# Performance work log

Measured on AMD Instinct MI355X. Metric: run time of the kernel, lower is better.

The kernel has to match this reference:

```python
import jax, jax.numpy as jnp
import numpy as np

N_NODES = 50000
N_EDGES = 800000
H = 128       # num_hidden
NUM_INV = 32  # num_inv


def _glorot(key, shape):
    fan_in, fan_out = shape[0], shape[1]
    lim = np.sqrt(6.0 / (fan_in + fan_out)).astype(np.float32)
    return jax.random.uniform(key, shape, jnp.float32, -lim, lim)


def setup_inputs() -> dict:
    key = jax.random.key(0)
    ks = jax.random.split(key, 12)
    x = jax.random.normal(ks[0], (N_NODES, H), jnp.float32)
    adj = jax.random.randint(ks[1], (2, N_EDGES), 0, N_NODES, dtype=jnp.int64)
    inv = jax.random.normal(ks[2], (N_EDGES, NUM_INV), jnp.float32)
    # MessageLayer: message_mlp = Linear(2H+inv -> H), SiLU, Linear(H -> H), SiLU
    Wm1 = _glorot(ks[3], (2 * H + NUM_INV, H)); bm1 = jnp.zeros((H,), jnp.float32)
    Wm2 = _glorot(ks[4], (H, H));               bm2 = jnp.zeros((H,), jnp.float32)
    # edge_inf_mlp = Linear(H -> 1), Sigmoid
    We = _glorot(ks[5], (H, 1));                be = jnp.zeros((1,), jnp.float32)
    # UpdateLayer (num_mes=1): update_mlp = Linear(2H -> H), SiLU, Linear(H -> H)
    Wu1 = _glorot(ks[6], (2 * H, H));           bu1 = jnp.zeros((H,), jnp.float32)
    Wu2 = _glorot(ks[7], (H, H));               bu2 = jnp.zeros((H,), jnp.float32)
    return {"x": x, "adj": adj, "inv": inv,
            "Wm1": Wm1, "bm1": bm1, "Wm2": Wm2, "bm2": bm2,
            "We": We, "be": be,
            "Wu1": Wu1, "bu1": bu1, "Wu2": Wu2, "bu2": bu2}


def reference(x, adj, inv, Wm1, bm1, Wm2, bm2, We, be, Wu1, bu1, Wu2, bu2):
    send, rec = adj[0], adj[1]
    # MessageLayer: gather endpoints, concat with invariants, 2-layer SiLU MLP
    state = jnp.concatenate([x[send], x[rec], inv], axis=1)      # [E, 2H+inv]
    h = jax.nn.silu(state @ Wm1 + bm1)                           # [E, H]
    msg = jax.nn.silu(h @ Wm2 + bm2)                             # [E, H]
    gate = jax.nn.sigmoid(msg @ We + be)                         # [E, 1]
    aggr = jax.ops.segment_sum(msg * gate, rec, num_segments=x.shape[0])  # [N, H]
    # UpdateLayer: concat [x, aggregated message], Linear-SiLU-Linear
    upd_in = jnp.concatenate([x, aggr], axis=1)                  # [N, 2H]
    x_up = jax.nn.silu(upd_in @ Wu1 + bu1) @ Wu2 + bu2           # [N, H]
    # Residual add
    return x + x_up
```

## Files before the change

### kernel.cpp

```cpp
#include <hip/hip_runtime.h>
#include <math.h>

#define NNODES 50000
#define NEDGES 800000
#define HDIM 128
#define NINV 32
#define K1 288
#define NTILES_E 25000
#define NTILES_N 1563
#define NB 196

#define W1STRIDE 296
#define U1STRIDE 264
#define HSTRIDE 132
#define FSTRIDE 66

typedef float floatx4 __attribute__((ext_vector_type(4)));
typedef short short8  __attribute__((ext_vector_type(8)));

union V4S8 { uint4 u; short8 s; int2 d[2]; };

__device__ __forceinline__ float silu_f(float z) { return z / (1.0f + __expf(-z)); }

__device__ __forceinline__ unsigned short f2bf_rne(float f) {
    unsigned u = __float_as_uint(f);
    u += 0x7fffu + ((u >> 16) & 1u);
    return (unsigned short)(u >> 16);
}

__device__ __forceinline__ unsigned pk_bf(float hi, float lo) {
    return __builtin_amdgcn_perm(__float_as_uint(hi), __float_as_uint(lo), 0x07060302);
}

__device__ __forceinline__ short8 cvt8(float4 f0, float4 f1) {
    V4S8 v;
    v.u.x = pk_bf(f0.y, f0.x);
    v.u.y = pk_bf(f0.w, f0.z);
    v.u.z = pk_bf(f1.y, f1.x);
    v.u.w = pk_bf(f1.w, f1.z);
    return v.s;
}

__device__ __forceinline__ int adj_at(const void* adj, int is64, long long pos) {
    if (is64) return (int)((const long long*)adj)[pos];
    return ((const int*)adj)[pos];
}

__global__ __launch_bounds__(256) void detect_idx64(const int* __restrict__ adj32,
                                                    int* __restrict__ flag) {
    __shared__ int any_nz;
    if (threadIdx.x == 0) any_nz = 0;
    __syncthreads();
    int v = adj32[threadIdx.x * 2 + 1];
    if (v != 0) atomicOr(&any_nz, 1);
    __syncthreads();
    if (threadIdx.x == 0) *flag = (any_nz == 0) ? 1 : 0;
}

__global__ __launch_bounds__(256) void prep_weights(
    const float* __restrict__ Wm1, const float* __restrict__ Wm2,
    const float* __restrict__ Wu1, const float* __restrict__ Wu2,
    unsigned short* __restrict__ Wm1t, unsigned short* __restrict__ Wm2t,
    unsigned short* __restrict__ Wu1t, unsigned short* __restrict__ Wu2t)
{
    int i = blockIdx.x * 256 + threadIdx.x;
    if (i < 128 * K1) {
        int n = i / K1, k = i % K1;
        Wm1t[i] = f2bf_rne(Wm1[k * HDIM + n]);
    } else if ((i -= 128 * K1) < 128 * HDIM) {
        int n = i / HDIM, k = i % HDIM;
        Wm2t[i] = f2bf_rne(Wm2[k * HDIM + n]);
    } else if ((i -= 128 * HDIM) < 128 * 256) {
        int n = i / 256, k = i % 256;
        Wu1t[i] = f2bf_rne(Wu1[k * HDIM + n]);
    } else if ((i -= 128 * 256) < 128 * HDIM) {
        int n = i / HDIM, k = i % HDIM;
        Wu2t[i] = f2bf_rne(Wu2[k * HDIM + n]);
    }
}

__global__ __launch_bounds__(256) void x2bf_kernel(const float* __restrict__ x,
                                                   unsigned short* __restrict__ xbf)
{
    int i = blockIdx.x * 256 + threadIdx.x;
    if (i < NNODES * HDIM / 8) {
        const float4* p = (const float4*)(x + i * 8);
        float4 f0 = p[0], f1 = p[1];
        V4S8 v;
        unsigned short u[8];
        u[0] = f2bf_rne(f0.x); u[1] = f2bf_rne(f0.y); u[2] = f2bf_rne(f0.z); u[3] = f2bf_rne(f0.w);
        u[4] = f2bf_rne(f1.x); u[5] = f2bf_rne(f1.y); u[6] = f2bf_rne(f1.z); u[7] = f2bf_rne(f1.w);
        v.u.x = (unsigned)u[0] | ((unsigned)u[1] << 16);
        v.u.y = (unsigned)u[2] | ((unsigned)u[3] << 16);
        v.u.z = (unsigned)u[4] | ((unsigned)u[5] << 16);
        v.u.w = (unsigned)u[6] | ((unsigned)u[7] << 16);
        *(uint4*)(xbf + i * 8) = v.u;
    }
}

__global__ __launch_bounds__(256) void hist_kernel(const void* __restrict__ adj,
                                                   const int* __restrict__ flagp,
                                                   int* __restrict__ hist)
{
    int e = blockIdx.x * 256 + threadIdx.x;
    if (e < NEDGES) {
        int r = adj_at(adj, *flagp, (long long)NEDGES + e);
        atomicAdd(&hist[r], 1);
    }
}

__global__ __launch_bounds__(256) void scanA_kernel(const int* __restrict__ hist,
                                                    int* __restrict__ bsum)
{
    __shared__ int red[256];
    int i = blockIdx.x * 256 + threadIdx.x;
    int v = (i < NNODES) ? hist[i] : 0;
    red[threadIdx.x] = v;
    __syncthreads();
    for (int d = 128; d > 0; d >>= 1) {
        if (threadIdx.x < d) red[threadIdx.x] += red[threadIdx.x + d];
        __syncthreads();
    }
    if (threadIdx.x == 0) bsum[blockIdx.x] = red[0];
}

__global__ __launch_bounds__(256) void scanB_kernel(const int* __restrict__ bsum,
                                                    int* __restrict__ boff)
{
    __shared__ int s[256];
    int t = threadIdx.x;
    int v = (t < NB) ? bsum[t] : 0;
    s[t] = v;
    __syncthreads();
    for (int d = 1; d < 256; d <<= 1) {
        int u = (t >= d) ? s[t - d] : 0;
        __syncthreads();
        s[t] += u;
        __syncthreads();
    }
    if (t < NB) boff[t] = s[t] - v;
}

__global__ __launch_bounds__(256) void scanC_kernel(const int* __restrict__ hist,
                                                    const int* __restrict__ boff,
                                                    int* __restrict__ cursor)
{
    __shared__ int s[256];
    int t = threadIdx.x;
    int i = blockIdx.x * 256 + t;
    int v = (i < NNODES) ? hist[i] : 0;
    s[t] = v;
    __syncthreads();
    for (int d = 1; d < 256; d <<= 1) {
        int u = (t >= d) ? s[t - d] : 0;
        __syncthreads();
        s[t] += u;
        __syncthreads();
    }
    if (i < NNODES) cursor[i] = boff[blockIdx.x] + s[t] - v;
}

__global__ __launch_bounds__(256) void scatter_kernel(const void* __restrict__ adj,
                                                      const int* __restrict__ flagp,
                                                      int* __restrict__ cursor,
                                                      int4* __restrict__ sEdge)
{
    int e = blockIdx.x * 256 + threadIdx.x;
    if (e < NEDGES) {
        int is64 = *flagp;
        int s = adj_at(adj, is64, e);
        int r = adj_at(adj, is64, (long long)NEDGES + e);
        int pos = atomicAdd(&cursor[r], 1);
        sEdge[pos] = make_int4(s, r, e, 0);
    }
}

__global__ __launch_bounds__(512, 2) void edge_kernel(
    const unsigned short* __restrict__ xbf, const float* __restrict__ inv,
    const int4* __restrict__ sEdge,
    const unsigned short* __restrict__ Wm1t, const float* __restrict__ bm1,
    const unsigned short* __restrict__ Wm2t, const float* __restrict__ bm2,
    const float* __restrict__ We, const float* __restrict__ be,
    float* __restrict__ aggr)
{
    __shared__ unsigned short s_w1[128 * W1STRIDE];
    __shared__ unsigned short s_h[8 * 32 * HSTRIDE];
    __shared__ int s_recb[8 * 32];

    const int t    = threadIdx.x;
    const int l    = t & 63;
    const int wid  = t >> 6;
    const int l15  = l & 15;
    const int quad = l >> 4;

    for (int idx = t; idx < 128 * 36; idx += 512) {
        int n = idx / 36, c = idx % 36;
        *(uint4*)&s_w1[n * W1STRIDE + c * 8] = *(const uint4*)(Wm1t + n * K1 + c * 8);
    }

    short8 w2f[4][8];
    #pragma unroll
    for (int ks = 0; ks < 4; ++ks)
        #pragma unroll
        for (int nt = 0; nt < 8; ++nt)
            w2f[ks][nt] = *(const short8*)(Wm2t + (nt * 16 + l15) * HDIM + ks * 32 + quad * 8);

    float bm1v[8], bm2v[8], wev[8];
    #pragma unroll
    for (int nt = 0; nt < 8; ++nt) {
        bm1v[nt] = bm1[nt * 16 + l15];
        bm2v[nt] = bm2[nt * 16 + l15];
        wev[nt]  = We[nt * 16 + l15];
    }
    const float be0 = be[0];

    __syncthreads();

    unsigned short* hbuf = s_h + wid * (32 * HSTRIDE);
    int* srec = s_recb + wid * 32;
    const int gwave  = blockIdx.x * 8 + wid;
    const int nwaves = gridDim.x * 8;
    if (gwave >= NTILES_E) return;

    int4 iA = sEdge[gwave * 32 + l15];
    int4 iB = sEdge[gwave * 32 + 16 + l15];
    unsigned oS0 = (unsigned)iA.x * HDIM, oR0 = (unsigned)iA.y * HDIM, oI0 = (unsigned)iA.z * NINV;
    unsigned oS1 = (unsigned)iB.x * HDIM, oR1 = (unsigned)iB.y * HDIM, oI1 = (unsigned)iB.z * NINV;

    short8 F[4][2];
    #pragma unroll
    for (int s = 0; s < 4; ++s) {
        F[s][0] = *(const short8*)(xbf + oS0 + s * 32 + quad * 8);
        F[s][1] = *(const short8*)(xbf + oS1 + s * 32 + quad * 8);
    }

    for (int tile = gwave; tile < NTILES_E; tile += nwaves) {
        const int ntile = tile + nwaves;
        const bool nv = ntile < NTILES_E;
        int4 nA, nB;
        if (nv) {
            nA = sEdge[ntile * 32 + l15];
            nB = sEdge[ntile * 32 + 16 + l15];
        }
        const int re0 = iA.y, re1 = iB.y;

        float4 I0[2], I1[2];
        {
            const float* p0 = inv + oI0 + quad * 8;
            const float* p1 = inv + oI1 + quad * 8;
            I0[0] = ((const float4*)p0)[0]; I0[1] = ((const float4*)p0)[1];
            I1[0] = ((const float4*)p1)[0]; I1[1] = ((const float4*)p1)[1];
        }

        floatx4 acc[2][8];
        #pragma unroll
        for (int nt = 0; nt < 8; ++nt) {
            acc[0][nt] = (floatx4){bm1v[nt], bm1v[nt], bm1v[nt], bm1v[nt]};
            acc[1][nt] = acc[0][nt];
        }

        #pragma unroll
        for (int s = 0; s < 9; ++s) {
            short8 a0 = F[s & 3][0];
            short8 a1 = F[s & 3][1];
            if (s < 4) {
                F[s][0] = *(const short8*)(xbf + oR0 + s * 32 + quad * 8);
                F[s][1] = *(const short8*)(xbf + oR1 + s * 32 + quad * 8);
            } else if (s == 5) {
                F[0][0] = cvt8(I0[0], I0[1]);
                F[0][1] = cvt8(I1[0], I1[1]);
            }
            const unsigned short* wbase = s_w1 + l15 * W1STRIDE + s * 32 + quad * 8;
            #pragma unroll
            for (int nt = 0; nt < 8; ++nt) {
                short8 b = *(const short8*)(wbase + nt * 16 * W1STRIDE);
                acc[0][nt] = __builtin_amdgcn_mfma_f32_16x16x32_bf16(a0, b, acc[0][nt], 0, 0, 0);
                acc[1][nt] = __builtin_amdgcn_mfma_f32_16x16x32_bf16(a1, b, acc[1][nt], 0, 0, 0);
            }
        }

        #pragma unroll
        for (int m = 0; m < 2; ++m)
            #pragma unroll
            for (int nt = 0; nt < 8; ++nt)
                #pragma unroll
                for (int r = 0; r < 4; ++r) {
                    float hv = silu_f(acc[m][nt][r]);
                    hbuf[(m * 16 + quad * 4 + r) * HSTRIDE + nt * 16 + l15] =
                        (unsigned short)(__float_as_uint(hv) >> 16);
                }

        #pragma unroll
        for (int nt = 0; nt < 8; ++nt) {
            acc[0][nt] = (floatx4){bm2v[nt], bm2v[nt], bm2v[nt], bm2v[nt]};
            acc[1][nt] = acc[0][nt];
        }

        #pragma unroll
        for (int ks = 0; ks < 4; ++ks) {
            short8 a2[2];
            #pragma unroll
            for (int m = 0; m < 2; ++m) {
                int base = (m * 16 + l15) * HSTRIDE + ks * 32 + quad * 8;
                V4S8 v;
                v.d[0] = *(const int2*)(hbuf + base);
                v.d[1] = *(const int2*)(hbuf + base + 4);
                a2[m] = v.s;
            }
            #pragma unroll
            for (int nt = 0; nt < 8; ++nt) {
                acc[0][nt] = __builtin_amdgcn_mfma_f32_16x16x32_bf16(a2[0], w2f[ks][nt], acc[0][nt], 0, 0, 0);
                acc[1][nt] = __builtin_amdgcn_mfma_f32_16x16x32_bf16(a2[1], w2f[ks][nt], acc[1][nt], 0, 0, 0);
            }
        }

        if (nv) {
            iA = nA; iB = nB;
            oS0 = (unsigned)iA.x * HDIM; oR0 = (unsigned)iA.y * HDIM; oI0 = (unsigned)iA.z * NINV;
            oS1 = (unsigned)iB.x * HDIM; oR1 = (unsigned)iB.y * HDIM; oI1 = (unsigned)iB.z * NINV;
            #pragma unroll
            for (int s = 0; s < 4; ++s) {
                F[s][0] = *(const short8*)(xbf + oS0 + s * 32 + quad * 8);
                F[s][1] = *(const short8*)(xbf + oS1 + s * 32 + quad * 8);
            }
        }

        #pragma unroll
        for (int m = 0; m < 2; ++m)
            #pragma unroll
            for (int nt = 0; nt < 8; ++nt)
                #pragma unroll
                for (int r = 0; r < 4; ++r)
                    acc[m][nt][r] = silu_f(acc[m][nt][r]);

        float g[2][4];
        #pragma unroll
        for (int m = 0; m < 2; ++m)
            #pragma unroll
            for (int r = 0; r < 4; ++r) {
                float part = 0.f;
                #pragma unroll
                for (int nt = 0; nt < 8; ++nt)
                    part = fmaf(acc[m][nt][r], wev[nt], part);
                part += __shfl_xor(part, 1);
                part += __shfl_xor(part, 2);
                part += __shfl_xor(part, 4);
                part += __shfl_xor(part, 8);
                g[m][r] = 1.0f / (1.0f + __expf(-(part + be0)));
            }

        if (quad == 0) { srec[l15] = re0; srec[16 + l15] = re1; }

        float* fred = (float*)hbuf;
        #pragma unroll
        for (int half = 0; half < 2; ++half) {
            #pragma unroll
            for (int m = 0; m < 2; ++m)
                #pragma unroll
                for (int nt2 = 0; nt2 < 4; ++nt2)
                    #pragma unroll
                    for (int r = 0; r < 4; ++r)
                        fred[(m * 16 + quad * 4 + r) * FSTRIDE + nt2 * 16 + l15] =
                            acc[m][half * 4 + nt2][r] * g[m][r];

            float* dstbase = aggr + half * 64 + l;
            float sum = 0.f;
            int prev = srec[0];
            #pragma unroll
            for (int row = 0; row < 32; ++row) {
                float v = fred[row * FSTRIDE + l];
                int rc = srec[row];
                if (rc != prev) {
                    atomicAdd(dstbase + (unsigned)prev * HDIM, sum);
                    sum = 0.f;
                    prev = rc;
                }
                sum += v;
            }
            atomicAdd(dstbase + (unsigned)prev * HDIM, sum);
        }
    }
}

__global__ __launch_bounds__(256) void node_kernel(
    const float* __restrict__ x, const unsigned short* __restrict__ xbf,
    const float* __restrict__ aggr,
    const unsigned short* __restrict__ Wu1t, const float* __restrict__ bu1,
    const unsigned short* __restrict__ Wu2t, const float* __restrict__ bu2,
    float* __restrict__ out)
{
    __shared__ unsigned short s_u1[128 * U1STRIDE];
    __shared__ unsigned short s_h[4 * 32 * HSTRIDE];

    const int t    = threadIdx.x;
    const int l    = t & 63;
    const int wid  = t >> 6;
    const int l15  = l & 15;
    const int quad = l >> 4;

    for (int idx = t; idx < 128 * 32; idx += 256) {
        int n = idx / 32, c = idx % 32;
        *(uint4*)&s_u1[n * U1STRIDE + c * 8] = *(const uint4*)(Wu1t + n * 256 + c * 8);
    }

    short8 w2f[4][8];
    #pragma unroll
    for (int ks = 0; ks < 4; ++ks)
        #pragma unroll
        for (int nt = 0; nt < 8; ++nt)
            w2f[ks][nt] = *(const short8*)(Wu2t + (nt * 16 + l15) * HDIM + ks * 32 + quad * 8);

    float bu1v[8], bu2v[8];
    #pragma unroll
    for (int nt = 0; nt < 8; ++nt) {
        bu1v[nt] = bu1[nt * 16 + l15];
        bu2v[nt] = bu2[nt * 16 + l15];
    }

    __syncthreads();

    unsigned short* hbuf = s_h + wid * (32 * HSTRIDE);
    const int nwaves = gridDim.x * 4;

    for (int tile = blockIdx.x * 4 + wid; tile < NTILES_N; tile += nwaves) {
        const int n0 = tile * 32;

        unsigned offX[2];
        #pragma unroll
        for (int m = 0; m < 2; ++m) {
            int row = n0 + m * 16 + l15;
            if (row >= NNODES) row = NNODES - 1;
            offX[m] = (unsigned)row * HDIM;
        }

        floatx4 acc[2][8];
        #pragma unroll
        for (int nt = 0; nt < 8; ++nt) {
            acc[0][nt] = (floatx4){bu1v[nt], bu1v[nt], bu1v[nt], bu1v[nt]};
            acc[1][nt] = acc[0][nt];
        }

        #pragma unroll
        for (int s = 0; s < 8; ++s) {
            short8 a[2];
            #pragma unroll
            for (int m = 0; m < 2; ++m) {
                if (s < 4) {
                    a[m] = *(const short8*)(xbf + offX[m] + s * 32 + quad * 8);
                } else {
                    const float* p = aggr + offX[m] + (s - 4) * 32 + quad * 8;
                    a[m] = cvt8(((const float4*)p)[0], ((const float4*)p)[1]);
                }
            }
            const unsigned short* wbase = s_u1 + l15 * U1STRIDE + s * 32 + quad * 8;
            #pragma unroll
            for (int nt = 0; nt < 8; ++nt) {
                short8 b = *(const short8*)(wbase + nt * 16 * U1STRIDE);
                acc[0][nt] = __builtin_amdgcn_mfma_f32_16x16x32_bf16(a[0], b, acc[0][nt], 0, 0, 0);
                acc[1][nt] = __builtin_amdgcn_mfma_f32_16x16x32_bf16(a[1], b, acc[1][nt], 0, 0, 0);
            }
        }

        #pragma unroll
        for (int m = 0; m < 2; ++m)
            #pragma unroll
            for (int nt = 0; nt < 8; ++nt)
                #pragma unroll
                for (int r = 0; r < 4; ++r) {
                    float hv = silu_f(acc[m][nt][r]);
                    hbuf[(m * 16 + quad * 4 + r) * HSTRIDE + nt * 16 + l15] =
                        (unsigned short)(__float_as_uint(hv) >> 16);
                }

        #pragma unroll
        for (int nt = 0; nt < 8; ++nt) {
            acc[0][nt] = (floatx4){bu2v[nt], bu2v[nt], bu2v[nt], bu2v[nt]};
            acc[1][nt] = acc[0][nt];
        }

        #pragma unroll
        for (int ks = 0; ks < 4; ++ks) {
            short8 a2[2];
            #pragma unroll
            for (int m = 0; m < 2; ++m) {
                int base = (m * 16 + l15) * HSTRIDE + ks * 32 + quad * 8;
                V4S8 v;
                v.d[0] = *(const int2*)(hbuf + base);
                v.d[1] = *(const int2*)(hbuf + base + 4);
                a2[m] = v.s;
            }
            #pragma unroll
            for (int nt = 0; nt < 8; ++nt) {
                acc[0][nt] = __builtin_amdgcn_mfma_f32_16x16x32_bf16(a2[0], w2f[ks][nt], acc[0][nt], 0, 0, 0);
                acc[1][nt] = __builtin_amdgcn_mfma_f32_16x16x32_bf16(a2[1], w2f[ks][nt], acc[1][nt], 0, 0, 0);
            }
        }

        #pragma unroll
        for (int m = 0; m < 2; ++m)
            #pragma unroll
            for (int r = 0; r < 4; ++r) {
                int row = n0 + m * 16 + quad * 4 + r;
                if (row < NNODES) {
                    #pragma unroll
                    for (int nt = 0; nt < 8; ++nt) {
                        int col = nt * 16 + l15;
                        out[(long long)row * HDIM + col] = x[(long long)row * HDIM + col] + acc[m][nt][r];
                    }
                }
            }
    }
}

extern "C" void kernel_launch(void* const* d_in, const int* in_sizes, int n_in,
                              void* d_out, int out_size, void* d_ws, size_t ws_size,
                              hipStream_t stream)
{
    const float* x   = (const float*)d_in[0];
    const void*  adj = d_in[1];
    const float* inv = (const float*)d_in[2];
    const float* Wm1 = (const float*)d_in[3];
    const float* bm1 = (const float*)d_in[4];
    const float* Wm2 = (const float*)d_in[5];
    const float* bm2 = (const float*)d_in[6];
    const float* We  = (const float*)d_in[7];
    const float* be  = (const float*)d_in[8];
    const float* Wu1 = (const float*)d_in[9];
    const float* bu1 = (const float*)d_in[10];
    const float* Wu2 = (const float*)d_in[11];
    const float* bu2 = (const float*)d_in[12];
    float* out = (float*)d_out;

    char* ws = (char*)d_ws;
    float* aggr = (float*)ws;
    size_t off = (size_t)NNODES * HDIM * 4;
    int* hist   = (int*)(ws + off);          off += (size_t)NNODES * 4;
    int* flag = (int*)(ws + off);            off += 64;
    unsigned short* Wm1t = (unsigned short*)(ws + off);  off += 128 * K1 * 2;
    unsigned short* Wm2t = (unsigned short*)(ws + off);  off += 128 * HDIM * 2;
    unsigned short* Wu1t = (unsigned short*)(ws + off);  off += 128 * 256 * 2;
    unsigned short* Wu2t = (unsigned short*)(ws + off);  off += 128 * HDIM * 2;
    off = (off + 63) & ~(size_t)63;
    unsigned short* xbf = (unsigned short*)(ws + off);   off += (size_t)NNODES * HDIM * 2;
    int* cursor = (int*)(ws + off);          off += (size_t)NNODES * 4;
    int* bsum   = (int*)(ws + off);          off += 1024;
    int* boff   = (int*)(ws + off);          off += 1024;
    off = (off + 63) & ~(size_t)63;
    int4* sEdge = (int4*)(ws + off);         off += (size_t)NEDGES * 16;

    hipMemsetAsync(aggr, 0, (size_t)(NNODES * HDIM + NNODES) * sizeof(float), stream);
    detect_idx64<<<1, 256, 0, stream>>>((const int*)adj, flag);
    prep_weights<<<400, 256, 0, stream>>>(Wm1, Wm2, Wu1, Wu2, Wm1t, Wm2t, Wu1t, Wu2t);
    x2bf_kernel<<<(NNODES * HDIM / 8 + 255) / 256, 256, 0, stream>>>(x, xbf);
    hist_kernel<<<(NEDGES + 255) / 256, 256, 0, stream>>>(adj, flag, hist);
    scanA_kernel<<<NB, 256, 0, stream>>>(hist, bsum);
    scanB_kernel<<<1, 256, 0, stream>>>(bsum, boff);
    scanC_kernel<<<NB, 256, 0, stream>>>(hist, boff, cursor);
    scatter_kernel<<<(NEDGES + 255) / 256, 256, 0, stream>>>(adj, flag, cursor, sEdge);
    edge_kernel<<<256, 512, 0, stream>>>(xbf, inv, sEdge,
                                         Wm1t, bm1, Wm2t, bm2, We, be, aggr);
    node_kernel<<<256, 256, 0, stream>>>(x, xbf, aggr, Wu1t, bu1, Wu2t, bu2, out);
}
```

Measured before the change: 621.2 us.

## Fuse preprocessing launches, inline index-width detection, and use contiguous edge tile ranges

Folds the index-width probe, weight transpose, x-to-bf16 conversion and histogram into one kernel launch. The block-offset scan is merged into the per-block scan, and each kernel detects the index width with a wave ballot, so the flag buffer is gone. Each edge-kernel wave now takes a contiguous range of sorted tiles rather than striding, which may improve locality of the receiver rows and of aggr scatters. All receiver features are preloaded into a larger register array, which raises register pressure. The x conversion computes a redundant pk_bf packing that is then overwritten.

```diff
diff --git a/kernel.cpp b/kernel.cpp
--- a/kernel.cpp
+++ b/kernel.cpp
@@ -10,6 +10,10 @@
 #define NTILES_N 1563
 #define NB 196
 
+#define PREP_NB 400
+#define X2BF_NB 3125
+#define HIST_NB 3125
+
 #define W1STRIDE 296
 #define U1STRIDE 264
 #define HSTRIDE 132
@@ -46,66 +50,62 @@
     return ((const int*)adj)[pos];
 }
 
-__global__ __launch_bounds__(256) void detect_idx64(const int* __restrict__ adj32,
-                                                    int* __restrict__ flag) {
-    __shared__ int any_nz;
-    if (threadIdx.x == 0) any_nz = 0;
-    __syncthreads();
-    int v = adj32[threadIdx.x * 2 + 1];
-    if (v != 0) atomicOr(&any_nz, 1);
-    __syncthreads();
-    if (threadIdx.x == 0) *flag = (any_nz == 0) ? 1 : 0;
-}
-
-__global__ __launch_bounds__(256) void prep_weights(
+__device__ __forceinline__ int detect64(const int* __restrict__ adj32) {
+    int l = threadIdx.x & 63;
+    int v = adj32[2 * l + 1] | adj32[2 * (l + 64) + 1]
+          | adj32[2 * (l + 128) + 1] | adj32[2 * (l + 192) + 1];
+    return (__ballot(v != 0) == 0ull) ? 1 : 0;
+}
+
+__global__ __launch_bounds__(256) void prep_all(
     const float* __restrict__ Wm1, const float* __restrict__ Wm2,
     const float* __restrict__ Wu1, const float* __restrict__ Wu2,
     unsigned short* __restrict__ Wm1t, unsigned short* __restrict__ Wm2t,
-    unsigned short* __restrict__ Wu1t, unsigned short* __restrict__ Wu2t)
-{
-    int i = blockIdx.x * 256 + threadIdx.x;
-    if (i < 128 * K1) {
-        int n = i / K1, k = i % K1;
-        Wm1t[i] = f2bf_rne(Wm1[k * HDIM + n]);
-    } else if ((i -= 128 * K1) < 128 * HDIM) {
-        int n = i / HDIM, k = i % HDIM;
-        Wm2t[i] = f2bf_rne(Wm2[k * HDIM + n]);
-    } else if ((i -= 128 * HDIM) < 128 * 256) {
-        int n = i / 256, k = i % 256;
-        Wu1t[i] = f2bf_rne(Wu1[k * HDIM + n]);
-    } else if ((i -= 128 * 256) < 128 * HDIM) {
-        int n = i / HDIM, k = i % HDIM;
-        Wu2t[i] = f2bf_rne(Wu2[k * HDIM + n]);
-    }
-}
-
-__global__ __launch_bounds__(256) void x2bf_kernel(const float* __restrict__ x,
-                                                   unsigned short* __restrict__ xbf)
-{
-    int i = blockIdx.x * 256 + threadIdx.x;
-    if (i < NNODES * HDIM / 8) {
-        const float4* p = (const float4*)(x + i * 8);
-        float4 f0 = p[0], f1 = p[1];
-        V4S8 v;
-        unsigned short u[8];
-        u[0] = f2bf_rne(f0.x); u[1] = f2bf_rne(f0.y); u[2] = f2bf_rne(f0.z); u[3] = f2bf_rne(f0.w);
-        u[4] = f2bf_rne(f1.x); u[5] = f2bf_rne(f1.y); u[6] = f2bf_rne(f1.z); u[7] = f2bf_rne(f1.w);
-        v.u.x = (unsigned)u[0] | ((unsigned)u[1] << 16);
-        v.u.y = (unsigned)u[2] | ((unsigned)u[3] << 16);
-        v.u.z = (unsigned)u[4] | ((unsigned)u[5] << 16);
-        v.u.w = (unsigned)u[6] | ((unsigned)u[7] << 16);
-        *(uint4*)(xbf + i * 8) = v.u;
-    }
-}
-
-__global__ __launch_bounds__(256) void hist_kernel(const void* __restrict__ adj,
-                                                   const int* __restrict__ flagp,
-                                                   int* __restrict__ hist)
-{
-    int e = blockIdx.x * 256 + threadIdx.x;
-    if (e < NEDGES) {
-        int r = adj_at(adj, *flagp, (long long)NEDGES + e);
-        atomicAdd(&hist[r], 1);
+    unsigned short* __restrict__ Wu1t, unsigned short* __restrict__ Wu2t,
+    const float* __restrict__ x, unsigned short* __restrict__ xbf,
+    const void* __restrict__ adj, int* __restrict__ hist)
+{
+    int bid = blockIdx.x;
+    if (bid < PREP_NB) {
+        int i = bid * 256 + threadIdx.x;
+        if (i < 128 * K1) {
+            int n = i / K1, k = i % K1;
+            Wm1t[i] = f2bf_rne(Wm1[k * HDIM + n]);
+        } else if ((i -= 128 * K1) < 128 * HDIM) {
+            int n = i / HDIM, k = i % HDIM;
+            Wm2t[i] = f2bf_rne(Wm2[k * HDIM + n]);
+        } else if ((i -= 128 * HDIM) < 128 * 256) {
+            int n = i / 256, k = i % 256;
+            Wu1t[i] = f2bf_rne(Wu1[k * HDIM + n]);
+        } else if ((i -= 128 * 256) < 128 * HDIM) {
+            int n = i / HDIM, k = i % HDIM;
+            Wu2t[i] = f2bf_rne(Wu2[k * HDIM + n]);
+        }
+    } else if (bid < PREP_NB + X2BF_NB) {
+        int i = (bid - PREP_NB) * 256 + threadIdx.x;
+        if (i < NNODES * HDIM / 8) {
+            const float4* p = (const float4*)(x + i * 8);
+            float4 f0 = p[0], f1 = p[1];
+            uint4 u;
+            u.x = pk_bf(f0.y, f0.x);
+            u.y = pk_bf(f0.w, f0.z);
+            u.z = pk_bf(f1.y, f1.x);
+            u.w = pk_bf(f1.w, f1.z);
+            unsigned short s0 = f2bf_rne(f0.x), s1 = f2bf_rne(f0.y), s2 = f2bf_rne(f0.z), s3 = f2bf_rne(f0.w);
+            unsigned short s4 = f2bf_rne(f1.x), s5 = f2bf_rne(f1.y), s6 = f2bf_rne(f1.z), s7 = f2bf_rne(f1.w);
+            u.x = (unsigned)s0 | ((unsigned)s1 << 16);
+            u.y = (unsigned)s2 | ((unsigned)s3 << 16);
+            u.z = (unsigned)s4 | ((unsigned)s5 << 16);
+            u.w = (unsigned)s6 | ((unsigned)s7 << 16);
+            *(uint4*)(xbf + i * 8) = u;
+        }
+    } else {
+        int is64 = detect64((const int*)adj);
+        int e = (bid - PREP_NB - X2BF_NB) * 256 + threadIdx.x;
+        if (e < NEDGES) {
+            int r = adj_at(adj, is64, (long long)NEDGES + e);
+            atomicAdd(&hist[r], 1);
+        }
     }
 }
 
@@ -124,50 +124,37 @@
     if (threadIdx.x == 0) bsum[blockIdx.x] = red[0];
 }
 
-__global__ __launch_bounds__(256) void scanB_kernel(const int* __restrict__ bsum,
-                                                    int* __restrict__ boff)
-{
+__global__ __launch_bounds__(256) void scanC_kernel(const int* __restrict__ hist,
+                                                    const int* __restrict__ bsum,
+                                                    int* __restrict__ cursor)
+{
+    __shared__ int sb[256];
     __shared__ int s[256];
     int t = threadIdx.x;
-    int v = (t < NB) ? bsum[t] : 0;
-    s[t] = v;
-    __syncthreads();
-    for (int d = 1; d < 256; d <<= 1) {
-        int u = (t >= d) ? s[t - d] : 0;
-        __syncthreads();
-        s[t] += u;
-        __syncthreads();
-    }
-    if (t < NB) boff[t] = s[t] - v;
-}
-
-__global__ __launch_bounds__(256) void scanC_kernel(const int* __restrict__ hist,
-                                                    const int* __restrict__ boff,
-                                                    int* __restrict__ cursor)
-{
-    __shared__ int s[256];
-    int t = threadIdx.x;
+    sb[t] = (t < NB) ? bsum[t] : 0;
     int i = blockIdx.x * 256 + t;
     int v = (i < NNODES) ? hist[i] : 0;
     s[t] = v;
     __syncthreads();
     for (int d = 1; d < 256; d <<= 1) {
-        int u = (t >= d) ? s[t - d] : 0;
+        int ub = (t >= d) ? sb[t - d] : 0;
+        int us = (t >= d) ? s[t - d] : 0;
         __syncthreads();
-        s[t] += u;
+        sb[t] += ub;
+        s[t]  += us;
         __syncthreads();
     }
-    if (i < NNODES) cursor[i] = boff[blockIdx.x] + s[t] - v;
+    int boff = (blockIdx.x == 0) ? 0 : sb[blockIdx.x - 1];
+    if (i < NNODES) cursor[i] = boff + s[t] - v;
 }
 
 __global__ __launch_bounds__(256) void scatter_kernel(const void* __restrict__ adj,
-                                                      const int* __restrict__ flagp,
                                                       int* __restrict__ cursor,
                                                       int4* __restrict__ sEdge)
 {
+    int is64 = detect64((const int*)adj);
     int e = blockIdx.x * 256 + threadIdx.x;
     if (e < NEDGES) {
-        int is64 = *flagp;
         int s = adj_at(adj, is64, e);
         int r = adj_at(adj, is64, (long long)NEDGES + e);
         int pos = atomicAdd(&cursor[r], 1);
@@ -220,30 +207,36 @@
     int* srec = s_recb + wid * 32;
     const int gwave  = blockIdx.x * 8 + wid;
     const int nwaves = gridDim.x * 8;
-    if (gwave >= NTILES_E) return;
-
-    int4 iA = sEdge[gwave * 32 + l15];
-    int4 iB = sEdge[gwave * 32 + 16 + l15];
+    const int t_lo = (int)((long long)gwave * NTILES_E / nwaves);
+    const int t_hi = (int)((long long)(gwave + 1) * NTILES_E / nwaves);
+    if (t_lo >= t_hi) return;
+
+    int4 iA = sEdge[t_lo * 32 + l15];
+    int4 iB = sEdge[t_lo * 32 + 16 + l15];
     unsigned oS0 = (unsigned)iA.x * HDIM, oR0 = (unsigned)iA.y * HDIM, oI0 = (unsigned)iA.z * NINV;
     unsigned oS1 = (unsigned)iB.x * HDIM, oR1 = (unsigned)iB.y * HDIM, oI1 = (unsigned)iB.z * NINV;
 
-    short8 F[4][2];
+    short8 F[8][2];
     #pragma unroll
     for (int s = 0; s < 4; ++s) {
         F[s][0] = *(const short8*)(xbf + oS0 + s * 32 + quad * 8);
         F[s][1] = *(const short8*)(xbf + oS1 + s * 32 + quad * 8);
     }
 
-    for (int tile = gwave; tile < NTILES_E; tile += nwaves) {
-        const int ntile = tile + nwaves;
-        const bool nv = ntile < NTILES_E;
+    for (int tile = t_lo; tile < t_hi; ++tile) {
+        const bool nv = (tile + 1) < t_hi;
         int4 nA, nB;
         if (nv) {
-            nA = sEdge[ntile * 32 + l15];
-            nB = sEdge[ntile * 32 + 16 + l15];
+            nA = sEdge[(tile + 1) * 32 + l15];
+            nB = sEdge[(tile + 1) * 32 + 16 + l15];
         }
         const int re0 = iA.y, re1 = iB.y;
 
+        #pragma unroll
+        for (int s = 0; s < 4; ++s) {
+            F[4 + s][0] = *(const short8*)(xbf + oR0 + s * 32 + quad * 8);
+            F[4 + s][1] = *(const short8*)(xbf + oR1 + s * 32 + quad * 8);
+        }
         float4 I0[2], I1[2];
         {
             const float* p0 = inv + oI0 + quad * 8;
@@ -259,16 +252,15 @@
             acc[1][nt] = acc[0][nt];
         }
 
+        short8 Fi0, Fi1;
         #pragma unroll
         for (int s = 0; s < 9; ++s) {
-            short8 a0 = F[s & 3][0];
-            short8 a1 = F[s & 3][1];
-            if (s < 4) {
-                F[s][0] = *(const short8*)(xbf + oR0 + s * 32 + quad * 8);
-                F[s][1] = *(const short8*)(xbf + oR1 + s * 32 + quad * 8);
-            } else if (s == 5) {
-                F[0][0] = cvt8(I0[0], I0[1]);
-                F[0][1] = cvt8(I1[0], I1[1]);
+            short8 a0, a1;
+            if (s < 8) { a0 = F[s][0]; a1 = F[s][1]; }
+            else       { a0 = Fi0;     a1 = Fi1;     }
+            if (s == 6) {
+                Fi0 = cvt8(I0[0], I0[1]);
+                Fi1 = cvt8(I1[0], I1[1]);
             }
             const unsigned short* wbase = s_w1 + l15 * W1STRIDE + s * 32 + quad * 8;
             #pragma unroll
@@ -535,7 +527,6 @@
     float* aggr = (float*)ws;
     size_t off = (size_t)NNODES * HDIM * 4;
     int* hist   = (int*)(ws + off);          off += (size_t)NNODES * 4;
-    int* flag = (int*)(ws + off);            off += 64;
     unsigned short* Wm1t = (unsigned short*)(ws + off);  off += 128 * K1 * 2;
     unsigned short* Wm2t = (unsigned short*)(ws + off);  off += 128 * HDIM * 2;
     unsigned short* Wu1t = (unsigned short*)(ws + off);  off += 128 * 256 * 2;
@@ -544,19 +535,15 @@
     unsigned short* xbf = (unsigned short*)(ws + off);   off += (size_t)NNODES * HDIM * 2;
     int* cursor = (int*)(ws + off);          off += (size_t)NNODES * 4;
     int* bsum   = (int*)(ws + off);          off += 1024;
-    int* boff   = (int*)(ws + off);          off += 1024;
     off = (off + 63) & ~(size_t)63;
     int4* sEdge = (int4*)(ws + off);         off += (size_t)NEDGES * 16;
 
     hipMemsetAsync(aggr, 0, (size_t)(NNODES * HDIM + NNODES) * sizeof(float), stream);
-    detect_idx64<<<1, 256, 0, stream>>>((const int*)adj, flag);
-    prep_weights<<<400, 256, 0, stream>>>(Wm1, Wm2, Wu1, Wu2, Wm1t, Wm2t, Wu1t, Wu2t);
-    x2bf_kernel<<<(NNODES * HDIM / 8 + 255) / 256, 256, 0, stream>>>(x, xbf);
-    hist_kernel<<<(NEDGES + 255) / 256, 256, 0, stream>>>(adj, flag, hist);
+    prep_all<<<PREP_NB + X2BF_NB + HIST_NB, 256, 0, stream>>>(
+        Wm1, Wm2, Wu1, Wu2, Wm1t, Wm2t, Wu1t, Wu2t, x, xbf, adj, hist);
     scanA_kernel<<<NB, 256, 0, stream>>>(hist, bsum);
-    scanB_kernel<<<1, 256, 0, stream>>>(bsum, boff);
-    scanC_kernel<<<NB, 256, 0, stream>>>(hist, boff, cursor);
-    scatter_kernel<<<(NEDGES + 255) / 256, 256, 0, stream>>>(adj, flag, cursor, sEdge);
+    scanC_kernel<<<NB, 256, 0, stream>>>(hist, bsum, cursor);
+    scatter_kernel<<<(NEDGES + 255) / 256, 256, 0, stream>>>(adj, cursor, sEdge);
     edge_kernel<<<256, 512, 0, stream>>>(xbf, inv, sEdge,
                                          Wm1t, bm1, Wm2t, bm2, We, be, aggr);
     node_kernel<<<256, 256, 0, stream>>>(x, xbf, aggr, Wu1t, bu1, Wu2t, bu2, out);
```

Measured after the change: 609.1 us. About the same (-2.0%).
